# Optimization experiments

Measured on AMD Instinct MI355X. Metric: run time of the kernel, lower is better.

The kernel has to match this reference:

```python
import jax, jax.numpy as jnp
import numpy as np

B, N, C, K = 32, 4096, 768, 64

def setup_inputs() -> dict:
    key = jax.random.key(0)
    k1, k2 = jax.random.split(key)
    x = jax.random.normal(k1, (B, N, C), dtype=jnp.float32)
    # nn.Linear(in_dim, K, bias=False) weight has shape [K, in_dim]
    W = jax.random.normal(k2, (K, C), dtype=jnp.float32) * (1.0 / np.sqrt(C))
    return {"x_bhwc": x, "W": W}

def reference(x_bhwc, W):
    # logits: [B, N, K]
    logits = jnp.einsum('bnc,kc->bnk', x_bhwc, W)
    # softmax over spatial dim N (dim=1)
    attn = jax.nn.softmax(logits, axis=1)
    # weighted sum over N -> [B, K, C]
    tokens = jnp.einsum('bnk,bnc->bkc', attn, x_bhwc)
    return tokens
```

## Files before the change

### kernel.cpp

```cpp
#include <hip/hip_runtime.h>
#include <hip/hip_bf16.h>

#define Bdim 32
#define Ndim 4096
#define Cdim 768
#define Kdim 64

typedef float f32x4 __attribute__((ext_vector_type(4)));
typedef short s16x8 __attribute__((ext_vector_type(8)));
typedef __bf16 bf16x8 __attribute__((ext_vector_type(8)));

__device__ __forceinline__ short f2bf(float f) {
  return __builtin_bit_cast(short, (__bf16)f);
}
__device__ __forceinline__ float bf2f(short s) {
  return (float)__builtin_bit_cast(__bf16, s);
}
__device__ __forceinline__ f32x4 MFMA(s16x8 a, s16x8 b, f32x4 c) {
  return __builtin_amdgcn_mfma_f32_16x16x32_bf16(
      __builtin_bit_cast(bf16x8, a), __builtin_bit_cast(bf16x8, b), c, 0, 0, 0);
}

__global__ void k0_wcvt(const float* __restrict__ W, short* __restrict__ Wr) {
  int idx = blockIdx.x * 256 + threadIdx.x;
  if (idx >= Kdim * Cdim / 8) return;
  int k = idx / (Cdim / 8), c8 = idx % (Cdim / 8);
  int cs = c8 >> 2, g = c8 & 3;
  int t = k >> 4, i = k & 15;
  const float* src = W + (size_t)k * Cdim + c8 * 8;
  s16x8 v;
#pragma unroll
  for (int e = 0; e < 8; ++e) v[e] = f2bf(src[e]);
  *(s16x8*)(Wr + ((((size_t)cs * 4 + t) * 4 + g) * 16 + i) * 8) = v;
}

__global__ __launch_bounds__(256) void k1_logits(
    const float* __restrict__ x, const short* __restrict__ Wr,
    short* __restrict__ P, float* __restrict__ ps) {
  const int blk = blockIdx.x;
  const int b = blk >> 6;
  const int ntile = blk & 63;
  const int tid = threadIdx.x;
  const int w = tid >> 6;
  const int l = tid & 63;
  const int g = l >> 4, i = l & 15;

  const float* xrow = x + (size_t)(b * Ndim + ntile * 64 + w * 16 + i) * Cdim;
  f32x4 acc[4] = {};

  for (int grp = 0; grp < 6; ++grp) {
    const int cbase = grp * 128 + g * 8;
    f32x4 xv[8];
    s16x8 wv[4][4];
#pragma unroll
    for (int s = 0; s < 4; ++s) {
      const f32x4* ap = (const f32x4*)(xrow + cbase + s * 32);
      xv[2 * s] = ap[0];
      xv[2 * s + 1] = ap[1];
    }
#pragma unroll
    for (int s = 0; s < 4; ++s) {
#pragma unroll
      for (int t = 0; t < 4; ++t) {
        wv[s][t] = *(const s16x8*)(
            Wr + ((((size_t)(grp * 4 + s) * 4 + t) * 4 + g) * 16 + i) * 8);
      }
    }
#pragma unroll
    for (int s = 0; s < 4; ++s) {
      s16x8 af;
#pragma unroll
      for (int e = 0; e < 4; ++e) af[e] = f2bf(xv[2 * s][e]);
#pragma unroll
      for (int e = 0; e < 4; ++e) af[4 + e] = f2bf(xv[2 * s + 1][e]);
#pragma unroll
      for (int t = 0; t < 4; ++t) acc[t] = MFMA(af, wv[s][t], acc[t]);
    }
  }

  short* Pb = P + (size_t)b * (Ndim * Kdim);
  float sv[4];
#pragma unroll
  for (int t = 0; t < 4; ++t) {
    sv[t] = 0.f;
#pragma unroll
    for (int r = 0; r < 4; ++r) {
      int n = ntile * 64 + w * 16 + g * 4 + r;
      int k = t * 16 + i;
      short hv = f2bf(__expf(acc[t][r]));
      Pb[(n >> 3) * 512 + k * 8 + (n & 7)] = hv;
      sv[t] += bf2f(hv);
    }
    sv[t] += __shfl_xor(sv[t], 16);
    sv[t] += __shfl_xor(sv[t], 32);
  }
  __shared__ float rs[4][4][16];
  if (g == 0) {
#pragma unroll
    for (int t = 0; t < 4; ++t) rs[w][t][i] = sv[t];
  }
  __syncthreads();
  if (w == 0 && g == 0) {
#pragma unroll
    for (int t = 0; t < 4; ++t) {
      float S = rs[0][t][i] + rs[1][t][i] + rs[2][t][i] + rs[3][t][i];
      ps[((size_t)b * 64 + ntile) * 64 + t * 16 + i] = S;
    }
  }
}

__global__ __launch_bounds__(256) void k2b_combine(
    const float* __restrict__ ps, float* __restrict__ invd) {
  const int b = blockIdx.x;
  const int t = threadIdx.x;
  const int k = t & 63, nt4 = t >> 6;
  float S = 0.f;
#pragma unroll
  for (int j = 0; j < 16; ++j)
    S += ps[((size_t)b * 64 + nt4 * 16 + j) * 64 + k];
  __shared__ float ss[4][64];
  ss[nt4][k] = S;
  __syncthreads();
  if (nt4 == 0) {
    float St = ss[0][k] + ss[1][k] + ss[2][k] + ss[3][k];
    invd[b * 64 + k] = 1.f / St;
  }
}

#define CT 48
#define NCH 128
#define NQ 4
#define BUFO (CT * 128)
__device__ __forceinline__ int swz(int c) {
  return ((((c >> 3) ^ c) & 7) << 4);
}
__global__ __launch_bounds__(256) void k3_tokens(
    const float* __restrict__ x, const short* __restrict__ P,
    float* __restrict__ part) {
  __shared__ short xs[2 * BUFO];
  char* xsb = (char*)xs;
  const int blk = blockIdx.x;
  const int q = blk & 3;
  const int ct = (blk >> 2) & 15;
  const int b = blk >> 6;
  const int tid = threadIdx.x;
  const int w = tid >> 6, l = tid & 63, g = l >> 4, i = l & 15;

  const float* xb = x + (size_t)b * Ndim * Cdim;
  const short* Pb = P + (size_t)b * (Ndim * Kdim);

  f32x4 acc[3] = {};

#define LOADX(ch, buf)                                                        \
  do {                                                                        \
    const int n0_ = (ch) * NCH;                                               \
    _Pragma("unroll") for (int uu = 0; uu < 3; ++uu) {                        \
      int u_ = tid + uu * 256;                                                \
      int n_ = u_ / 6, c8_ = u_ % 6;                                          \
      const f32x4* src_ =                                                     \
          (const f32x4*)(xb + (size_t)(n0_ + n_) * Cdim + ct * CT + c8_ * 8); \
      buf[uu][0] = src_[0];                                                   \
      buf[uu][1] = src_[1];                                                   \
    }                                                                         \
  } while (0)

#define LOADL(ch, lvb)                                                        \
  do {                                                                        \
    const int nb8_ = (ch) * 16;                                               \
    _Pragma("unroll") for (int ns = 0; ns < 4; ++ns) {                        \
      lvb[ns] = *(const s16x8*)(Pb + (size_t)(nb8_ + ns * 4 + g) * 512 +      \
                                (w * 16 + i) * 8);                            \
    }                                                                         \
  } while (0)

#define STORELDS(base, buf)                                                   \
  do {                                                                        \
    _Pragma("unroll") for (int uu = 0; uu < 3; ++uu) {                        \
      int u_ = tid + uu * 256;                                                \
      int n_ = u_ / 6, c8_ = u_ % 6;                                          \
      _Pragma("unroll") for (int e = 0; e < 8; ++e) {                         \
        int c_ = c8_ * 8 + e;                                                 \
        float fv_ = (e < 4) ? buf[uu][0][e] : buf[uu][1][e - 4];              \
        *(short*)(xsb + (base) + c_ * 256 + ((2 * n_) ^ swz(c_))) = f2bf(fv_);\
      }                                                                       \
    }                                                                         \
  } while (0)

#define COMPUTE(base, lvb)                                                    \
  do {                                                                        \
    _Pragma("unroll") for (int ns = 0; ns < 4; ++ns) {                        \
      _Pragma("unroll") for (int cs = 0; cs < 3; ++cs) {                      \
        const int c_ = cs * 16 + i;                                           \
        s16x8 bfr_ = *(const s16x8*)(xsb + (base) + c_ * 256 +                \
                                     ((ns * 64 + g * 16) ^ swz(c_)));         \
        acc[cs] = MFMA(lvb[ns], bfr_, acc[cs]);                               \
      }                                                                       \
    }                                                                         \
  } while (0)

#define SOFT_BARRIER()                                                        \
  do {                                                                        \
    asm volatile("s_waitcnt lgkmcnt(0)" ::: "memory");                        \
    __builtin_amdgcn_s_barrier();                                             \
    __builtin_amdgcn_sched_barrier(0);                                        \
  } while (0)

  f32x4 stA[3][2], stB[3][2];
  s16x8 lvA[4], lvB[4];

  const int ch0 = q * 8;
  LOADX(ch0, stA);
  LOADL(ch0, lvA);
  LOADX(ch0 + 1, stB);
  LOADL(ch0 + 1, lvB);
  STORELDS(0, stA);
  SOFT_BARRIER();

  for (int c = 0; c < 8; c += 2) {
    if (c + 2 < 8) LOADX(ch0 + c + 2, stA);
    STORELDS(BUFO * 2, stB);
    COMPUTE(0, lvA);
    if (c + 2 < 8) LOADL(ch0 + c + 2, lvA);
    SOFT_BARRIER();
    if (c + 3 < 8) LOADX(ch0 + c + 3, stB);
    if (c + 2 < 8) STORELDS(0, stA);
    COMPUTE(BUFO * 2, lvB);
    if (c + 3 < 8) LOADL(ch0 + c + 3, lvB);
    SOFT_BARRIER();
  }

  float* pb = part + ((size_t)q * Bdim + b) * (Kdim * Cdim);
#pragma unroll
  for (int r = 0; r < 4; ++r) {
    const int k = w * 16 + g * 4 + r;
#pragma unroll
    for (int cs = 0; cs < 3; ++cs) {
      pb[(size_t)k * Cdim + ct * CT + cs * 16 + i] = acc[cs][r];
    }
  }
#undef LOADX
#undef LOADL
#undef STORELDS
#undef COMPUTE
#undef SOFT_BARRIER
}

#define QSTRIDE (Bdim * Kdim * Cdim / 4)
__global__ __launch_bounds__(256) void k4_reduce(
    const float* __restrict__ part, const float* __restrict__ invd,
    float* __restrict__ out) {
  const int idx = blockIdx.x * 256 + threadIdx.x;
  const f32x4* p = (const f32x4*)part;
  f32x4 s = p[idx] + p[idx + QSTRIDE] + p[idx + 2 * QSTRIDE] + p[idx + 3 * QSTRIDE];
  const float sc = invd[(idx * 4) / Cdim];
  ((f32x4*)out)[idx] = s * sc;
}

extern "C" void kernel_launch(void* const* d_in, const int* in_sizes, int n_in,
                              void* d_out, int out_size, void* d_ws, size_t ws_size,
                              hipStream_t stream) {
  const float* x = (const float*)d_in[0];
  const float* W = (const float*)d_in[1];
  float* out = (float*)d_out;
  char* ws = (char*)d_ws;

  short* Wb = (short*)ws;
  short* P = (short*)(ws + (1 << 17));
  char* after = ws + (1 << 17) + (size_t)Bdim * Ndim * Kdim * 2;
  float* psum = (float*)after;
  float* iv = psum + Bdim * 64 * 64;
  float* part = iv + Bdim * Kdim;

  hipLaunchKernelGGL(k0_wcvt, dim3(24), dim3(256), 0, stream, W, Wb);
  hipLaunchKernelGGL(k1_logits, dim3(Bdim * 64), dim3(256), 0, stream, x, Wb, P, psum);
  hipLaunchKernelGGL(k2b_combine, dim3(Bdim), dim3(256), 0, stream, psum, iv);
  hipLaunchKernelGGL(k3_tokens, dim3(Bdim * 16 * NQ), dim3(256), 0, stream, x, P, part);
  hipLaunchKernelGGL(k4_reduce, dim3(Bdim * Kdim * Cdim / 4 / 256), dim3(256), 0, stream,
                     part, iv, out);
}
```

Baseline: 211.4 us.

## Retile token kernel to 256-wide C slabs with full K per block

Restructures the attention-weighted sum kernel so each block covers a 256-channel slab, all 64 K outputs and 512 rows of N, with a 4x4 accumulator tile per wave. This raises MFMA work per LDS read and cuts how often the softmax weights are re-read across channel blocks. LDS stores now pack two N rows per 32-bit write. The N split grows from 4 to 8, which doubles the partial buffer the reduce kernel must read and the workspace it needs. Weight fragments are now loaded inside the compute step instead of being prefetched.

```diff
diff --git a/kernel.cpp b/kernel.cpp
--- a/kernel.cpp
+++ b/kernel.cpp
@@ -127,73 +127,81 @@
   }
 }
 
-#define CT 48
-#define NCH 128
-#define NQ 4
-#define BUFO (CT * 128)
+#define NQ2 8
+#define CSLAB 256
+#define KST 64
+#define STEPS 8
+#define BUFSH (CSLAB * KST)
 __device__ __forceinline__ int swz(int c) {
   return ((((c >> 3) ^ c) & 7) << 4);
 }
 __global__ __launch_bounds__(256) void k3_tokens(
     const float* __restrict__ x, const short* __restrict__ P,
     float* __restrict__ part) {
-  __shared__ short xs[2 * BUFO];
+  __shared__ short xs[2 * BUFSH];
   char* xsb = (char*)xs;
   const int blk = blockIdx.x;
-  const int q = blk & 3;
-  const int ct = (blk >> 2) & 15;
-  const int b = blk >> 6;
+  const int cb = blk % 3;
+  const int q = (blk / 3) & 7;
+  const int b = blk / 24;
   const int tid = threadIdx.x;
   const int w = tid >> 6, l = tid & 63, g = l >> 4, i = l & 15;
 
-  const float* xb = x + (size_t)b * Ndim * Cdim;
+  const float* xb = x + (size_t)b * Ndim * Cdim + cb * CSLAB;
   const short* Pb = P + (size_t)b * (Ndim * Kdim);
-
-  f32x4 acc[3] = {};
-
-#define LOADX(ch, buf)                                                        \
-  do {                                                                        \
-    const int n0_ = (ch) * NCH;                                               \
-    _Pragma("unroll") for (int uu = 0; uu < 3; ++uu) {                        \
+  const int n0 = q * 512;
+
+  f32x4 acc[4][4] = {};
+  f32x4 sr[4][4];
+
+#define LOADS(s)                                                              \
+  do {                                                                        \
+    _Pragma("unroll") for (int uu = 0; uu < 4; ++uu) {                        \
       int u_ = tid + uu * 256;                                                \
-      int n_ = u_ / 6, c8_ = u_ % 6;                                          \
-      const f32x4* src_ =                                                     \
-          (const f32x4*)(xb + (size_t)(n0_ + n_) * Cdim + ct * CT + c8_ * 8); \
-      buf[uu][0] = src_[0];                                                   \
-      buf[uu][1] = src_[1];                                                   \
+      int n2_ = (u_ >> 5) * 2, cu_ = u_ & 31;                                 \
+      const f32x4* p0_ =                                                      \
+          (const f32x4*)(xb + (size_t)(n0 + (s) * KST + n2_) * Cdim + cu_ * 8);\
+      const f32x4* p1_ =                                                      \
+          (const f32x4*)(xb + (size_t)(n0 + (s) * KST + n2_ + 1) * Cdim + cu_ * 8);\
+      sr[uu][0] = p0_[0];                                                     \
+      sr[uu][1] = p0_[1];                                                     \
+      sr[uu][2] = p1_[0];                                                     \
+      sr[uu][3] = p1_[1];                                                     \
     }                                                                         \
   } while (0)
 
-#define LOADL(ch, lvb)                                                        \
-  do {                                                                        \
-    const int nb8_ = (ch) * 16;                                               \
-    _Pragma("unroll") for (int ns = 0; ns < 4; ++ns) {                        \
-      lvb[ns] = *(const s16x8*)(Pb + (size_t)(nb8_ + ns * 4 + g) * 512 +      \
-                                (w * 16 + i) * 8);                            \
-    }                                                                         \
-  } while (0)
-
-#define STORELDS(base, buf)                                                   \
-  do {                                                                        \
-    _Pragma("unroll") for (int uu = 0; uu < 3; ++uu) {                        \
+#define WRITE(base)                                                           \
+  do {                                                                        \
+    _Pragma("unroll") for (int uu = 0; uu < 4; ++uu) {                        \
       int u_ = tid + uu * 256;                                                \
-      int n_ = u_ / 6, c8_ = u_ % 6;                                          \
+      int n2_ = (u_ >> 5) * 2, cu_ = u_ & 31;                                 \
       _Pragma("unroll") for (int e = 0; e < 8; ++e) {                         \
-        int c_ = c8_ * 8 + e;                                                 \
-        float fv_ = (e < 4) ? buf[uu][0][e] : buf[uu][1][e - 4];              \
-        *(short*)(xsb + (base) + c_ * 256 + ((2 * n_) ^ swz(c_))) = f2bf(fv_);\
+        int c_ = cu_ * 8 + e;                                                 \
+        float v0_ = (e < 4) ? sr[uu][0][e] : sr[uu][1][e - 4];                \
+        float v1_ = (e < 4) ? sr[uu][2][e] : sr[uu][3][e - 4];                \
+        unsigned pk_ = (unsigned)(unsigned short)f2bf(v0_) |                  \
+                       ((unsigned)(unsigned short)f2bf(v1_) << 16);           \
+        *(unsigned*)(xsb + (base) + c_ * 128 + ((2 * n2_) ^ swz(c_))) = pk_;  \
       }                                                                       \
     }                                                                         \
   } while (0)
 
-#define COMPUTE(base, lvb)                                                    \
-  do {                                                                        \
-    _Pragma("unroll") for (int ns = 0; ns < 4; ++ns) {                        \
-      _Pragma("unroll") for (int cs = 0; cs < 3; ++cs) {                      \
-        const int c_ = cs * 16 + i;                                           \
-        s16x8 bfr_ = *(const s16x8*)(xsb + (base) + c_ * 256 +                \
-                                     ((ns * 64 + g * 16) ^ swz(c_)));         \
-        acc[cs] = MFMA(lvb[ns], bfr_, acc[cs]);                               \
+#define COMPUTE(base, s)                                                      \
+  do {                                                                        \
+    s16x8 A_[4][2];                                                           \
+    _Pragma("unroll") for (int kt = 0; kt < 4; ++kt)                          \
+    _Pragma("unroll") for (int ns = 0; ns < 2; ++ns)                          \
+        A_[kt][ns] = *(const s16x8*)(                                         \
+            Pb + ((size_t)(n0 / 8 + (s) * 8 + ns * 4 + g)) * 512 +            \
+            (kt * 16 + i) * 8);                                               \
+    _Pragma("unroll") for (int ct = 0; ct < 4; ++ct) {                        \
+      const int c_ = w * 64 + ct * 16 + i;                                    \
+      _Pragma("unroll") for (int ns = 0; ns < 2; ++ns) {                      \
+        const int noff_ = ns * 32 + g * 8;                                    \
+        s16x8 B_ = *(const s16x8*)(xsb + (base) + c_ * 128 +                  \
+                                   ((2 * noff_) ^ swz(c_)));                  \
+        _Pragma("unroll") for (int kt = 0; kt < 4; ++kt)                      \
+            acc[kt][ct] = MFMA(A_[kt][ns], B_, acc[kt][ct]);                  \
       }                                                                       \
     }                                                                         \
   } while (0)
@@ -205,42 +213,34 @@
     __builtin_amdgcn_sched_barrier(0);                                        \
   } while (0)
 
-  f32x4 stA[3][2], stB[3][2];
-  s16x8 lvA[4], lvB[4];
-
-  const int ch0 = q * 8;
-  LOADX(ch0, stA);
-  LOADL(ch0, lvA);
-  LOADX(ch0 + 1, stB);
-  LOADL(ch0 + 1, lvB);
-  STORELDS(0, stA);
+  LOADS(0);
+  WRITE(0);
   SOFT_BARRIER();
-
-  for (int c = 0; c < 8; c += 2) {
-    if (c + 2 < 8) LOADX(ch0 + c + 2, stA);
-    STORELDS(BUFO * 2, stB);
-    COMPUTE(0, lvA);
-    if (c + 2 < 8) LOADL(ch0 + c + 2, lvA);
+#pragma unroll 2
+  for (int s = 0; s < STEPS; ++s) {
+    const int cur = (s & 1) * (BUFSH * 2);
+    const int nxt = ((s + 1) & 1) * (BUFSH * 2);
+    if (s + 1 < STEPS) LOADS(s + 1);
+    COMPUTE(cur, s);
+    if (s + 1 < STEPS) WRITE(nxt);
     SOFT_BARRIER();
-    if (c + 3 < 8) LOADX(ch0 + c + 3, stB);
-    if (c + 2 < 8) STORELDS(0, stA);
-    COMPUTE(BUFO * 2, lvB);
-    if (c + 3 < 8) LOADL(ch0 + c + 3, lvB);
-    SOFT_BARRIER();
   }
 
   float* pb = part + ((size_t)q * Bdim + b) * (Kdim * Cdim);
 #pragma unroll
-  for (int r = 0; r < 4; ++r) {
-    const int k = w * 16 + g * 4 + r;
-#pragma unroll
-    for (int cs = 0; cs < 3; ++cs) {
-      pb[(size_t)k * Cdim + ct * CT + cs * 16 + i] = acc[cs][r];
-    }
-  }
-#undef LOADX
-#undef LOADL
-#undef STORELDS
+  for (int kt = 0; kt < 4; ++kt) {
+#pragma unroll
+    for (int r = 0; r < 4; ++r) {
+      const int k = kt * 16 + g * 4 + r;
+#pragma unroll
+      for (int ct = 0; ct < 4; ++ct) {
+        const int c = cb * CSLAB + w * 64 + ct * 16 + i;
+        pb[(size_t)k * Cdim + c] = acc[kt][ct][r];
+      }
+    }
+  }
+#undef LOADS
+#undef WRITE
 #undef COMPUTE
 #undef SOFT_BARRIER
 }
@@ -251,7 +251,9 @@
     float* __restrict__ out) {
   const int idx = blockIdx.x * 256 + threadIdx.x;
   const f32x4* p = (const f32x4*)part;
-  f32x4 s = p[idx] + p[idx + QSTRIDE] + p[idx + 2 * QSTRIDE] + p[idx + 3 * QSTRIDE];
+  f32x4 s = p[idx] + p[idx + QSTRIDE];
+#pragma unroll
+  for (int j = 2; j < NQ2; ++j) s += p[idx + (size_t)j * QSTRIDE];
   const float sc = invd[(idx * 4) / Cdim];
   ((f32x4*)out)[idx] = s * sc;
 }
@@ -274,7 +276,7 @@
   hipLaunchKernelGGL(k0_wcvt, dim3(24), dim3(256), 0, stream, W, Wb);
   hipLaunchKernelGGL(k1_logits, dim3(Bdim * 64), dim3(256), 0, stream, x, Wb, P, psum);
   hipLaunchKernelGGL(k2b_combine, dim3(Bdim), dim3(256), 0, stream, psum, iv);
-  hipLaunchKernelGGL(k3_tokens, dim3(Bdim * 16 * NQ), dim3(256), 0, stream, x, P, part);
+  hipLaunchKernelGGL(k3_tokens, dim3(Bdim * 3 * NQ2), dim3(256), 0, stream, x, P, part);
   hipLaunchKernelGGL(k4_reduce, dim3(Bdim * Kdim * Cdim / 4 / 256), dim3(256), 0, stream,
                      part, iv, out);
 }
```

Result: slower. 220.5 us (+4.3%).
